# Kernel optimization log

Measured on AMD Instinct MI355X. Metric: run time of the kernel, lower is better.

## Reference

```python
import jax, jax.numpy as jnp
import numpy as np

N = 50000
E = 600000
F_IN = 128      # float features (in_channels - 1)
CE = 8          # cell embedding dim
D_IN = F_IN + CE  # 136
C = 128         # out_channels
NUM_CELLS = 854
NEG_SLOPE = 0.2
LN_EPS = 1e-5


def _gat_layer(x, src, dst, W, a_src, a_dst, b):
    """PyG GATConv, heads=1, concat=False, add_self_loops already in src/dst.
    x: [N, Din]; src/dst: [Etot]; W: [Din, C]; a_src/a_dst: [C]; b: [C].
    """
    h = x @ W                               # [N, C]
    alpha_src = h @ a_src                   # [N]
    alpha_dst = h @ a_dst                   # [N]
    e = jax.nn.leaky_relu(alpha_src[src] + alpha_dst[dst], NEG_SLOPE)  # [Etot]
    # segment softmax over edges sharing a destination node
    m = jax.ops.segment_max(e, dst, num_segments=N)    # [N] (every node has a self-loop)
    ex = jnp.exp(e - m[dst])                           # [Etot]
    denom = jax.ops.segment_sum(ex, dst, num_segments=N)  # [N]
    alpha = ex / denom[dst]                            # [Etot]
    out = jax.ops.segment_sum(h[src] * alpha[:, None], dst, num_segments=N)  # [N, C]
    return out + b


def _layer_norm(x, g, b):
    mu = jnp.mean(x, axis=-1, keepdims=True)
    var = jnp.var(x, axis=-1, keepdims=True)
    return (x - mu) * jax.lax.rsqrt(var + LN_EPS) * g + b


def setup_inputs() -> dict:
    key = jax.random.key(0)
    ks = jax.random.split(key, 12)
    x_base = jax.random.normal(ks[0], (N, F_IN), dtype=jnp.float32)
    cell_ids = jax.random.randint(ks[1], (N,), 0, NUM_CELLS, dtype=jnp.int64)
    edge_index = jax.random.randint(ks[2], (2, E), 0, N, dtype=jnp.int64)
    s = 0.05
    cell_emb = jax.random.normal(ks[3], (NUM_CELLS, CE), dtype=jnp.float32)
    W1 = jax.random.normal(ks[4], (D_IN, C), dtype=jnp.float32) * s
    a_src1 = jax.random.normal(ks[5], (C,), dtype=jnp.float32) * s
    a_dst1 = jax.random.normal(ks[6], (C,), dtype=jnp.float32) * s
    b1 = jnp.zeros((C,), dtype=jnp.float32)
    ln_g = jnp.ones((C,), dtype=jnp.float32)
    ln_b = jnp.zeros((C,), dtype=jnp.float32)
    W2 = jax.random.normal(ks[7], (C, C), dtype=jnp.float32) * s
    a_src2 = jax.random.normal(ks[8], (C,), dtype=jnp.float32) * s
    a_dst2 = jax.random.normal(ks[9], (C,), dtype=jnp.float32) * s
    b2 = jnp.zeros((C,), dtype=jnp.float32)
    return {
        "x_base": x_base, "cell_ids": cell_ids, "edge_index": edge_index,
        "cell_emb": cell_emb,
        "W1": W1, "a_src1": a_src1, "a_dst1": a_dst1, "b1": b1,
        "ln_g": ln_g, "ln_b": ln_b,
        "W2": W2, "a_src2": a_src2, "a_dst2": a_dst2, "b2": b2,
    }


def reference(x_base, cell_ids, edge_index, cell_emb,
              W1, a_src1, a_dst1, b1, ln_g, ln_b,
              W2, a_src2, a_dst2, b2):
    # embed cell ids and concat (equiv. to x[:, :-1] + Embedding(x[:, -1]))
    x = jnp.concatenate([x_base, cell_emb[cell_ids]], axis=1)   # [N, 136]
    # PyG GATConv adds self-loops internally
    loops = jnp.arange(N, dtype=edge_index.dtype)
    src = jnp.concatenate([edge_index[0], loops])
    dst = jnp.concatenate([edge_index[1], loops])
    # layer 1 + LN + ELU (dropout inactive in eval mode)
    x = _gat_layer(x, src, dst, W1, a_src1, a_dst1, b1)
    x = jax.nn.elu(_layer_norm(x, ln_g, ln_b))
    # layer 2 (no norm/activation on last layer)
    x = _gat_layer(x, src, dst, W2, a_src2, a_dst2, b2)
    return x
```

## Files before the change

kernel.cpp:

```cpp
#include <hip/hip_runtime.h>
#include <hip/hip_fp16.h>
#include <cstdint>
#include <cstddef>

#define NEG_SLOPE 0.2f
#define LN_EPS 1e-5f

constexpr int BS = 256;
constexpr int EPT = 8;
constexpr int SUBCAP = 96;
constexpr int STRIDE = 96;

typedef _Float16 f16x8 __attribute__((ext_vector_type(8)));
typedef float f32x4 __attribute__((ext_vector_type(4)));

__device__ __forceinline__ void agg_half8(
    const char* hbB, int idk, float wk, int qbase, int hoff, int l4, float acc[8])
{
    f16x8 hv[8];
    #pragma unroll
    for (int i = 0; i < 8; ++i) {
        int si = __shfl(idk, qbase + hoff + i);
        hv[i] = *(const f16x8*)(hbB + ((size_t)si << 8) + l4 * 16);
    }
    #pragma unroll
    for (int i = 0; i < 8; ++i) {
        float wi = __shfl(wk, qbase + hoff + i);
        #pragma unroll
        for (int c = 0; c < 8; ++c)
            acc[c] = fmaf(wi, (float)hv[i][c], acc[c]);
    }
}

__global__ __launch_bounds__(256) void k_init(
    const int* __restrict__ esrc, const int* __restrict__ edst,
    unsigned int* __restrict__ gb, int* __restrict__ bcnt,
    const float* __restrict__ W1, const float* __restrict__ W2,
    _Float16* __restrict__ Wt1, _Float16* __restrict__ Wt2,
    int e, int nb, int nblk)
{
    int b = blockIdx.x;
    if (b < nblk) {
        __shared__ int lcnt[64];
        int tid = threadIdx.x;
        if (tid < 64) lcnt[tid] = 0;
        __syncthreads();
        int base = b * (BS * EPT) + tid;
        int sv[EPT], dl[EPT], bk[EPT], lp[EPT];
        #pragma unroll
        for (int u = 0; u < EPT; ++u) {
            int i = base + u * BS;
            bool ok = i < e;
            int ii = ok ? i : 0;
            sv[u] = esrc[ii];
            int d = edst[ii];
            dl[u] = d & 1023;
            bk[u] = ok ? (d >> 10) : -1;
        }
        #pragma unroll
        for (int u = 0; u < EPT; ++u)
            lp[u] = (bk[u] >= 0) ? atomicAdd(&lcnt[bk[u]], 1) : SUBCAP;
        __syncthreads();
        if (tid < nb) bcnt[b * nb + tid] = lcnt[tid] < SUBCAP ? lcnt[tid] : SUBCAP;
        #pragma unroll
        for (int u = 0; u < EPT; ++u)
            if (bk[u] >= 0 && lp[u] < SUBCAP)
                gb[((size_t)bk[u] * nblk + b) * SUBCAP + lp[u]] =
                    ((unsigned)dl[u] << 16) | (unsigned)sv[u];
    } else {
        int idx = (b - nblk) * BS + threadIdx.x;
        if (idx < 128 * 160) {
            int nn = idx / 160, k = idx - nn * 160;
            Wt1[idx] = (_Float16)((k < 136) ? W1[(size_t)k * 128 + nn] : 0.f);
        } else if (idx < 128 * 160 + 128 * 128) {
            int j = idx - 128 * 160;
            int nn = j >> 7, k = j & 127;
            Wt2[j] = (_Float16)W2[(size_t)k * 128 + nn];
        }
    }
}

__global__ __launch_bounds__(256) void k_csr_gemm1(
    const unsigned int* __restrict__ gb, const int* __restrict__ bcnt,
    int* __restrict__ cnt, unsigned short* __restrict__ sn,
    const float* __restrict__ x, const int* __restrict__ cid,
    const float* __restrict__ emb,
    const _Float16* __restrict__ Wt1,
    const float* __restrict__ a_src, const float* __restrict__ a_dst,
    _Float16* __restrict__ hb, float* __restrict__ as_, float* __restrict__ ad_,
    int n, int nb, int nblk)
{
    __shared__ float red[2][16][2][2];
    __shared__ int cl[1024];
    int b = blockIdx.x;

    if (b < nb) {
        int tid = threadIdx.x;
        #pragma unroll 4
        for (int i = tid; i < 1024; i += BS) cl[i] = 1;
        __syncthreads();
        for (int blk = tid; blk < nblk; blk += BS) {
            int c = bcnt[blk * nb + b];
            size_t gbase = ((size_t)b * nblk + blk) * SUBCAP;
            for (int j = 0; j < c; j += 8) {
                uint4 p0 = *(const uint4*)(gb + gbase + j);
                uint4 p1 = *(const uint4*)(gb + gbase + j + 4);
                unsigned pk[8] = {p0.x, p0.y, p0.z, p0.w, p1.x, p1.y, p1.z, p1.w};
                int slot[8];
                #pragma unroll
                for (int k = 0; k < 8; ++k)
                    slot[k] = (j + k < c) ? atomicAdd(&cl[pk[k] >> 16], 1) : STRIDE;
                #pragma unroll
                for (int k = 0; k < 8; ++k)
                    if (slot[k] < STRIDE)
                        sn[((size_t)(b * 1024 + (int)(pk[k] >> 16))) * STRIDE + slot[k]] =
                            (unsigned short)(pk[k] & 0xFFFFu);
            }
        }
        __syncthreads();
        for (int i = tid; i < 1024; i += BS) {
            int node = b * 1024 + i;
            if (node < n) {
                int c = cl[i];
                cnt[node] = c < STRIDE ? c : STRIDE;
                sn[(size_t)node * STRIDE] = (unsigned short)node;
            }
        }
        return;
    }

    int idx = b - nb;
    int tid = threadIdx.x;
    int wave = tid >> 6, lane = tid & 63;
    int rg = wave >> 1, ch = wave & 1;
    int r15 = lane & 15, q = lane >> 4;
    int rowBase = idx * 32 + rg * 16;
    int colBase = ch * 64;
    int row = rowBase + r15;
    bool ok = row < n;
    int rl = ok ? row : n - 1;

    f32x4 acc[4] = {};
    const _Float16* Wp[4];
    #pragma unroll
    for (int s = 0; s < 4; ++s)
        Wp[s] = Wt1 + (size_t)(colBase + s * 16 + r15) * 160 + q * 8;
    const float* Xp = x + (size_t)rl * 128 + q * 8;

    #pragma unroll
    for (int k0 = 0; k0 < 128; k0 += 32) {
        f16x8 wv[4];
        #pragma unroll
        for (int s = 0; s < 4; ++s) wv[s] = *(const f16x8*)(Wp[s] + k0);
        float4 xlo = *(const float4*)(Xp + k0);
        float4 xhi = *(const float4*)(Xp + k0 + 4);
        f16x8 xv;
        xv[0] = (_Float16)xlo.x; xv[1] = (_Float16)xlo.y;
        xv[2] = (_Float16)xlo.z; xv[3] = (_Float16)xlo.w;
        xv[4] = (_Float16)xhi.x; xv[5] = (_Float16)xhi.y;
        xv[6] = (_Float16)xhi.z; xv[7] = (_Float16)xhi.w;
        #pragma unroll
        for (int s = 0; s < 4; ++s)
            acc[s] = __builtin_amdgcn_mfma_f32_16x16x32_f16(wv[s], xv, acc[s], 0, 0, 0);
    }
    {
        f16x8 wv[4];
        #pragma unroll
        for (int s = 0; s < 4; ++s) wv[s] = *(const f16x8*)(Wp[s] + 128);
        f16x8 xv;
        #pragma unroll
        for (int j = 0; j < 8; ++j) xv[j] = (_Float16)0.f;
        if (q == 0) {
            const float* er = emb + (size_t)cid[rl] * 8;
            float4 e0 = *(const float4*)er;
            float4 e1 = *(const float4*)(er + 4);
            xv[0] = (_Float16)e0.x; xv[1] = (_Float16)e0.y;
            xv[2] = (_Float16)e0.z; xv[3] = (_Float16)e0.w;
            xv[4] = (_Float16)e1.x; xv[5] = (_Float16)e1.y;
            xv[6] = (_Float16)e1.z; xv[7] = (_Float16)e1.w;
        }
        #pragma unroll
        for (int s = 0; s < 4; ++s)
            acc[s] = __builtin_amdgcn_mfma_f32_16x16x32_f16(wv[s], xv, acc[s], 0, 0, 0);
    }

    float vs = 0.f, vd = 0.f;
    #pragma unroll
    for (int s = 0; s < 4; ++s) {
        float4 as4 = *(const float4*)&a_src[colBase + s * 16 + q * 4];
        float4 ad4 = *(const float4*)&a_dst[colBase + s * 16 + q * 4];
        f32x4 d = acc[s];
        vs += d[0]*as4.x + d[1]*as4.y + d[2]*as4.z + d[3]*as4.w;
        vd += d[0]*ad4.x + d[1]*ad4.y + d[2]*ad4.z + d[3]*ad4.w;
        if (ok) {
            ushort4 u;
            u.x = __half_as_ushort(__float2half_rn(d[0]));
            u.y = __half_as_ushort(__float2half_rn(d[1]));
            u.z = __half_as_ushort(__float2half_rn(d[2]));
            u.w = __half_as_ushort(__float2half_rn(d[3]));
            *(ushort4*)&hb[(size_t)row * 128 + colBase + s * 16 + q * 4] = u;
        }
    }
    vs += __shfl_xor(vs, 16); vs += __shfl_xor(vs, 32);
    vd += __shfl_xor(vd, 16); vd += __shfl_xor(vd, 32);
    if (q == 0) { red[rg][r15][ch][0] = vs; red[rg][r15][ch][1] = vd; }
    __syncthreads();
    if (ch == 0 && q == 0 && ok) {
        as_[row] = red[rg][r15][0][0] + red[rg][r15][1][0];
        ad_[row] = red[rg][r15][0][1] + red[rg][r15][1][1];
    }
}

__global__ __launch_bounds__(512, 4) void k_agg1_gemm2(
    const _Float16* __restrict__ h1, const unsigned short* __restrict__ sn,
    const int* __restrict__ cnt, const float* __restrict__ as1,
    const float* __restrict__ ad1, const float* __restrict__ b1,
    const float* __restrict__ lng, const float* __restrict__ lnb,
    const _Float16* __restrict__ Wt2,
    const float* __restrict__ a_src2, const float* __restrict__ a_dst2,
    _Float16* __restrict__ h2, float* __restrict__ as2, float* __restrict__ ad2,
    int nn)
{
    __shared__ _Float16 yt[32][144];
    __shared__ float red[2][16][4][2];
    int t = blockIdx.x;
    int tid = threadIdx.x;
    int wave = tid >> 6, lane = tid & 63;
    int l4 = lane & 15, q = lane >> 4;
    int qg = wave * 4 + q;
    int node = t * 32 + qg;
    bool valid = node < nn;
    const char* hbB = (const char*)h1;
    int qbase = lane & 48;

    int len = 0; float adv = 0.f;
    if (valid) {
        len = cnt[node];
        len = len < STRIDE ? len : STRIDE;
        adv = ad1[node];
    }
    int start = valid ? node * STRIDE : 0;

    int id0 = sn[start + l4], id1 = sn[start + 16 + l4], id2 = sn[start + 32 + l4];
    id0 = (l4      < len) ? id0 : 0;
    id1 = (l4 + 16 < len) ? id1 : 0;
    id2 = (l4 + 32 < len) ? id2 : 0;
    float t0 = as1[id0] + adv; t0 = t0 > 0.f ? t0 : NEG_SLOPE * t0;
    float t1 = as1[id1] + adv; t1 = t1 > 0.f ? t1 : NEG_SLOPE * t1;
    float t2 = as1[id2] + adv; t2 = t2 > 0.f ? t2 : NEG_SLOPE * t2;
    float w0 = (l4      < len) ? __expf(fminf(t0, 70.f)) : 0.f;
    float w1 = (l4 + 16 < len) ? __expf(fminf(t1, 70.f)) : 0.f;
    float w2 = (l4 + 32 < len) ? __expf(fminf(t2, 70.f)) : 0.f;
    float wsum = w0 + w1 + w2;

    float acc[8] = {0.f, 0.f, 0.f, 0.f, 0.f, 0.f, 0.f, 0.f};
    agg_half8(hbB, id0, w0, qbase, 0, l4, acc);
    agg_half8(hbB, id0, w0, qbase, 8, l4, acc);
    if (len > 16) {
        agg_half8(hbB, id1, w1, qbase, 0, l4, acc);
        agg_half8(hbB, id1, w1, qbase, 8, l4, acc);
    }
    if (len > 32) {
        agg_half8(hbB, id2, w2, qbase, 0, l4, acc);
        agg_half8(hbB, id2, w2, qbase, 8, l4, acc);
    }
    for (int c = 48; c < len; c += 16) {
        int idk = sn[start + c + l4];
        bool a = (c + l4 < len);
        idk = a ? idk : 0;
        float tt = as1[idk] + adv; tt = tt > 0.f ? tt : NEG_SLOPE * tt;
        float wk = a ? __expf(fminf(tt, 70.f)) : 0.f;
        wsum += wk;
        agg_half8(hbB, idk, wk, qbase, 0, l4, acc);
        agg_half8(hbB, idk, wk, qbase, 8, l4, acc);
    }
    float dsum = wsum;
    dsum += __shfl_xor(dsum, 1); dsum += __shfl_xor(dsum, 2);
    dsum += __shfl_xor(dsum, 4); dsum += __shfl_xor(dsum, 8);

    if (valid) {
        float inv = 1.f / dsum;
        float4 b0 = *(const float4*)&b1[l4 * 8];
        float4 bb = *(const float4*)&b1[l4 * 8 + 4];
        float vv[8];
        vv[0] = acc[0] * inv + b0.x; vv[1] = acc[1] * inv + b0.y;
        vv[2] = acc[2] * inv + b0.z; vv[3] = acc[3] * inv + b0.w;
        vv[4] = acc[4] * inv + bb.x; vv[5] = acc[5] * inv + bb.y;
        vv[6] = acc[6] * inv + bb.z; vv[7] = acc[7] * inv + bb.w;

        float s1 = 0.f, s2 = 0.f;
        #pragma unroll
        for (int c = 0; c < 8; ++c) { s1 += vv[c]; s2 += vv[c] * vv[c]; }
        #pragma unroll
        for (int o = 1; o < 16; o <<= 1) {
            s1 += __shfl_xor(s1, o);
            s2 += __shfl_xor(s2, o);
        }
        float mean = s1 * (1.f / 128.f);
        float var  = s2 * (1.f / 128.f) - mean * mean;
        float r = rsqrtf(var + LN_EPS);
        float4 g0 = *(const float4*)&lng[l4 * 8];
        float4 g1 = *(const float4*)&lng[l4 * 8 + 4];
        float4 p0 = *(const float4*)&lnb[l4 * 8];
        float4 p1 = *(const float4*)&lnb[l4 * 8 + 4];
        float gg[8] = {g0.x, g0.y, g0.z, g0.w, g1.x, g1.y, g1.z, g1.w};
        float pp[8] = {p0.x, p0.y, p0.z, p0.w, p1.x, p1.y, p1.z, p1.w};
        f16x8 o;
        #pragma unroll
        for (int c = 0; c < 8; ++c) {
            float u = (vv[c] - mean) * r * gg[c] + pp[c];
            u = u > 0.f ? u : __expf(u) - 1.f;
            o[c] = (_Float16)u;
        }
        *(f16x8*)&yt[qg][l4 * 8] = o;
    } else {
        f16x8 z;
        #pragma unroll
        for (int c = 0; c < 8; ++c) z[c] = (_Float16)0.f;
        *(f16x8*)&yt[qg][l4 * 8] = z;
    }
    __syncthreads();

    int rg = wave >> 2, cc = wave & 3;
    int r15 = l4;
    int row = t * 32 + rg * 16 + r15;
    bool ok = row < nn;

    f32x4 acc2[2] = {};
    const _Float16* Wp[2];
    #pragma unroll
    for (int s = 0; s < 2; ++s)
        Wp[s] = Wt2 + (size_t)(cc * 32 + s * 16 + r15) * 128 + q * 8;
    const _Float16* Yp = &yt[rg * 16 + r15][q * 8];

    #pragma unroll
    for (int k0 = 0; k0 < 128; k0 += 32) {
        f16x8 wv[2];
        #pragma unroll
        for (int s = 0; s < 2; ++s) wv[s] = *(const f16x8*)(Wp[s] + k0);
        f16x8 xv = *(const f16x8*)(Yp + k0);
        #pragma unroll
        for (int s = 0; s < 2; ++s)
            acc2[s] = __builtin_amdgcn_mfma_f32_16x16x32_f16(wv[s], xv, acc2[s], 0, 0, 0);
    }

    float vs = 0.f, vd = 0.f;
    #pragma unroll
    for (int s = 0; s < 2; ++s) {
        float4 as4 = *(const float4*)&a_src2[cc * 32 + s * 16 + q * 4];
        float4 ad4 = *(const float4*)&a_dst2[cc * 32 + s * 16 + q * 4];
        f32x4 d = acc2[s];
        vs += d[0]*as4.x + d[1]*as4.y + d[2]*as4.z + d[3]*as4.w;
        vd += d[0]*ad4.x + d[1]*ad4.y + d[2]*ad4.z + d[3]*ad4.w;
        if (ok) {
            ushort4 u;
            u.x = __half_as_ushort(__float2half_rn(d[0]));
            u.y = __half_as_ushort(__float2half_rn(d[1]));
            u.z = __half_as_ushort(__float2half_rn(d[2]));
            u.w = __half_as_ushort(__float2half_rn(d[3]));
            *(ushort4*)&h2[(size_t)row * 128 + cc * 32 + s * 16 + q * 4] = u;
        }
    }
    vs += __shfl_xor(vs, 16); vs += __shfl_xor(vs, 32);
    vd += __shfl_xor(vd, 16); vd += __shfl_xor(vd, 32);
    if (q == 0) { red[rg][r15][cc][0] = vs; red[rg][r15][cc][1] = vd; }
    __syncthreads();
    if (cc == 0 && q == 0 && ok) {
        as2[row] = red[rg][r15][0][0] + red[rg][r15][1][0]
                 + red[rg][r15][2][0] + red[rg][r15][3][0];
        ad2[row] = red[rg][r15][0][1] + red[rg][r15][1][1]
                 + red[rg][r15][2][1] + red[rg][r15][3][1];
    }
}

__global__ __launch_bounds__(256, 4) void k_agg2(
    const _Float16* __restrict__ hb, const unsigned short* __restrict__ sn,
    const int* __restrict__ cnt, const float* __restrict__ as_,
    const float* __restrict__ ad_, const float* __restrict__ bias,
    float* __restrict__ out, int n_nodes)
{
    int tid = threadIdx.x;
    int wave = tid >> 6, lane = tid & 63;
    int l4 = lane & 15, q = lane >> 4;
    int node = blockIdx.x * 16 + wave * 4 + q;
    if (node >= n_nodes) return;
    int len = cnt[node];
    len = len < STRIDE ? len : STRIDE;
    int start = node * STRIDE;
    int qbase = lane & 48;
    float adv = ad_[node];
    const char* hbB = (const char*)hb;

    int id0 = sn[start + l4], id1 = sn[start + 16 + l4], id2 = sn[start + 32 + l4];
    id0 = (l4      < len) ? id0 : 0;
    id1 = (l4 + 16 < len) ? id1 : 0;
    id2 = (l4 + 32 < len) ? id2 : 0;
    float t0 = as_[id0] + adv; t0 = t0 > 0.f ? t0 : NEG_SLOPE * t0;
    float t1 = as_[id1] + adv; t1 = t1 > 0.f ? t1 : NEG_SLOPE * t1;
    float t2 = as_[id2] + adv; t2 = t2 > 0.f ? t2 : NEG_SLOPE * t2;
    float w0 = (l4      < len) ? __expf(fminf(t0, 70.f)) : 0.f;
    float w1 = (l4 + 16 < len) ? __expf(fminf(t1, 70.f)) : 0.f;
    float w2 = (l4 + 32 < len) ? __expf(fminf(t2, 70.f)) : 0.f;
    float wsum = w0 + w1 + w2;

    float acc[8] = {0.f, 0.f, 0.f, 0.f, 0.f, 0.f, 0.f, 0.f};
    agg_half8(hbB, id0, w0, qbase, 0, l4, acc);
    agg_half8(hbB, id0, w0, qbase, 8, l4, acc);
    if (len > 16) {
        agg_half8(hbB, id1, w1, qbase, 0, l4, acc);
        agg_half8(hbB, id1, w1, qbase, 8, l4, acc);
    }
    if (len > 32) {
        agg_half8(hbB, id2, w2, qbase, 0, l4, acc);
        agg_half8(hbB, id2, w2, qbase, 8, l4, acc);
    }
    for (int c = 48; c < len; c += 16) {
        int idk = sn[start + c + l4];
        bool a = (c + l4 < len);
        idk = a ? idk : 0;
        float tt = as_[idk] + adv; tt = tt > 0.f ? tt : NEG_SLOPE * tt;
        float wk = a ? __expf(fminf(tt, 70.f)) : 0.f;
        wsum += wk;
        agg_half8(hbB, idk, wk, qbase, 0, l4, acc);
        agg_half8(hbB, idk, wk, qbase, 8, l4, acc);
    }
    float dsum = wsum;
    dsum += __shfl_xor(dsum, 1); dsum += __shfl_xor(dsum, 2);
    dsum += __shfl_xor(dsum, 4); dsum += __shfl_xor(dsum, 8);

    float inv = 1.f / dsum;
    float4 b0 = *(const float4*)&bias[l4 * 8];
    float4 b1 = *(const float4*)&bias[l4 * 8 + 4];
    float4 o0 = make_float4(acc[0]*inv + b0.x, acc[1]*inv + b0.y,
                            acc[2]*inv + b0.z, acc[3]*inv + b0.w);
    float4 o1 = make_float4(acc[4]*inv + b1.x, acc[5]*inv + b1.y,
                            acc[6]*inv + b1.z, acc[7]*inv + b1.w);
    *(float4*)(out + (size_t)node * 128 + l4 * 8)     = o0;
    *(float4*)(out + (size_t)node * 128 + l4 * 8 + 4) = o1;
}


extern "C" void kernel_launch(void* const* d_in, const int* in_sizes, int n_in,
                              void* d_out, int out_size, void* d_ws, size_t ws_size,
                              hipStream_t stream) {
    const float* x_base   = (const float*)d_in[0];
    const int*   cell_ids = (const int*)d_in[1];
    const int*   eidx     = (const int*)d_in[2];
    const float* cell_emb = (const float*)d_in[3];
    const float* W1     = (const float*)d_in[4];
    const float* a_src1 = (const float*)d_in[5];
    const float* a_dst1 = (const float*)d_in[6];
    const float* b1     = (const float*)d_in[7];
    const float* ln_g   = (const float*)d_in[8];
    const float* ln_b   = (const float*)d_in[9];
    const float* W2     = (const float*)d_in[10];
    const float* a_src2 = (const float*)d_in[11];
    const float* a_dst2 = (const float*)d_in[12];
    const float* b2     = (const float*)d_in[13];

    const int N = in_sizes[0] / 128;
    const int E = in_sizes[2] / 2;

    const int* esrc = eidx;
    const int* edst = eidx + E;

    const int NB   = (N + 1023) >> 10;
    const int NBLK = (E + BS * EPT - 1) / (BS * EPT);

    auto align = [](size_t v) { return (v + 255) & ~(size_t)255; };
    char* p = (char*)d_ws;
    int*   cnt    = (int*)p;   p += align((size_t)N * 4);
    unsigned short* sn = (unsigned short*)p; p += align((size_t)N * STRIDE * 2 + 64);
    unsigned int* gb = (unsigned int*)p; p += align((size_t)NB * NBLK * SUBCAP * 4);
    int*   bcnt   = (int*)p;   p += align((size_t)NBLK * NB * 4);
    _Float16* h1  = (_Float16*)p; p += align((size_t)N * 128 * 2);
    _Float16* h2  = (_Float16*)p; p += align((size_t)N * 128 * 2);
    _Float16* Wt1 = (_Float16*)p; p += align((size_t)128 * 160 * 2);
    _Float16* Wt2 = (_Float16*)p; p += align((size_t)128 * 128 * 2);
    float* as1    = (float*)p; p += align((size_t)N * 4);
    float* ad1    = (float*)p; p += align((size_t)N * 4);
    float* as2    = (float*)p; p += align((size_t)N * 4);
    float* ad2    = (float*)p; p += align((size_t)N * 4);
    (void)ws_size; (void)n_in; (void)out_size;

    const int nbG = (N + 31) / 32;
    const int wblocks = (128 * 160 + 128 * 128 + BS - 1) / BS;

    k_init<<<NBLK + wblocks, BS, 0, stream>>>(
        esrc, edst, gb, bcnt, W1, W2, Wt1, Wt2, E, NB, NBLK);
    k_csr_gemm1<<<NB + nbG, BS, 0, stream>>>(
        gb, bcnt, cnt, sn, x_base, cell_ids, cell_emb, Wt1,
        a_src1, a_dst1, h1, as1, ad1, N, NB, NBLK);
    k_agg1_gemm2<<<nbG, 512, 0, stream>>>(
        h1, sn, cnt, as1, ad1, b1, ln_g, ln_b, Wt2,
        a_src2, a_dst2, h2, as2, ad2, N);
    k_agg2<<<(N + 15) / 16, BS, 0, stream>>>(
        h2, sn, cnt, as2, ad2, b2, (float*)d_out, N);
}
```

Baseline: 205.9 us.

## Sort nodes by degree within 1024-node chunks to balance aggregation waves

Each CSR-building block now builds a histogram of node in-degrees and counting-sorts its 1024 nodes by degree into a permutation array. The two aggregation kernels index nodes through this permutation, so the quarter-waves within a wave and block handle nodes of similar degree, which cuts divergence from per-lane loop lengths. In exchange it adds a serial prefix scan, shared-memory atomics and an extra indirection. It also scatters writes to h2/as2/ad2/out, losing contiguous row stores, and launches grids padded up to the chunk size.

```diff
diff --git a/kernel.cpp b/kernel.cpp
--- a/kernel.cpp
+++ b/kernel.cpp
@@ -10,6 +10,7 @@
 constexpr int EPT = 8;
 constexpr int SUBCAP = 96;
 constexpr int STRIDE = 96;
+constexpr int NBINS = 104;
 
 typedef _Float16 f16x8 __attribute__((ext_vector_type(8)));
 typedef float f32x4 __attribute__((ext_vector_type(4)));
@@ -83,6 +84,7 @@
 __global__ __launch_bounds__(256) void k_csr_gemm1(
     const unsigned int* __restrict__ gb, const int* __restrict__ bcnt,
     int* __restrict__ cnt, unsigned short* __restrict__ sn,
+    unsigned short* __restrict__ perm,
     const float* __restrict__ x, const int* __restrict__ cid,
     const float* __restrict__ emb,
     const _Float16* __restrict__ Wt1,
@@ -92,12 +94,15 @@
 {
     __shared__ float red[2][16][2][2];
     __shared__ int cl[1024];
+    __shared__ int hist[NBINS];
+    __shared__ int hbase[NBINS];
     int b = blockIdx.x;
 
     if (b < nb) {
         int tid = threadIdx.x;
         #pragma unroll 4
         for (int i = tid; i < 1024; i += BS) cl[i] = 1;
+        if (tid < NBINS) hist[tid] = 0;
         __syncthreads();
         for (int blk = tid; blk < nblk; blk += BS) {
             int c = bcnt[blk * nb + b];
@@ -120,11 +125,26 @@
         __syncthreads();
         for (int i = tid; i < 1024; i += BS) {
             int node = b * 1024 + i;
+            int c = cl[i];
+            int len = (node < n) ? (c < STRIDE ? c : STRIDE) : 0;
             if (node < n) {
-                int c = cl[i];
-                cnt[node] = c < STRIDE ? c : STRIDE;
+                cnt[node] = len;
                 sn[(size_t)node * STRIDE] = (unsigned short)node;
             }
+            atomicAdd(&hist[len], 1);
+        }
+        __syncthreads();
+        if (tid == 0) {
+            int run = 0;
+            for (int k = 0; k < NBINS; ++k) { hbase[k] = run; run += hist[k]; }
+        }
+        __syncthreads();
+        for (int i = tid; i < 1024; i += BS) {
+            int node = b * 1024 + i;
+            int c = cl[i];
+            int len = (node < n) ? (c < STRIDE ? c : STRIDE) : 0;
+            int pos = atomicAdd(&hbase[len], 1);
+            perm[b * 1024 + pos] = (node < n) ? (unsigned short)node : (unsigned short)0xFFFF;
         }
         return;
     }
@@ -213,7 +233,8 @@
 
 __global__ __launch_bounds__(512, 4) void k_agg1_gemm2(
     const _Float16* __restrict__ h1, const unsigned short* __restrict__ sn,
-    const int* __restrict__ cnt, const float* __restrict__ as1,
+    const int* __restrict__ cnt, const unsigned short* __restrict__ perm,
+    const float* __restrict__ as1,
     const float* __restrict__ ad1, const float* __restrict__ b1,
     const float* __restrict__ lng, const float* __restrict__ lnb,
     const _Float16* __restrict__ Wt2,
@@ -228,7 +249,7 @@
     int wave = tid >> 6, lane = tid & 63;
     int l4 = lane & 15, q = lane >> 4;
     int qg = wave * 4 + q;
-    int node = t * 32 + qg;
+    int node = perm[t * 32 + qg];
     bool valid = node < nn;
     const char* hbB = (const char*)h1;
     int qbase = lane & 48;
@@ -323,8 +344,8 @@
 
     int rg = wave >> 2, cc = wave & 3;
     int r15 = l4;
-    int row = t * 32 + rg * 16 + r15;
-    bool ok = row < nn;
+    int onode = perm[t * 32 + rg * 16 + r15];
+    bool ok = onode < nn;
 
     f32x4 acc2[2] = {};
     const _Float16* Wp[2];
@@ -358,7 +379,7 @@
             u.y = __half_as_ushort(__float2half_rn(d[1]));
             u.z = __half_as_ushort(__float2half_rn(d[2]));
             u.w = __half_as_ushort(__float2half_rn(d[3]));
-            *(ushort4*)&h2[(size_t)row * 128 + cc * 32 + s * 16 + q * 4] = u;
+            *(ushort4*)&h2[(size_t)onode * 128 + cc * 32 + s * 16 + q * 4] = u;
         }
     }
     vs += __shfl_xor(vs, 16); vs += __shfl_xor(vs, 32);
@@ -366,23 +387,24 @@
     if (q == 0) { red[rg][r15][cc][0] = vs; red[rg][r15][cc][1] = vd; }
     __syncthreads();
     if (cc == 0 && q == 0 && ok) {
-        as2[row] = red[rg][r15][0][0] + red[rg][r15][1][0]
-                 + red[rg][r15][2][0] + red[rg][r15][3][0];
-        ad2[row] = red[rg][r15][0][1] + red[rg][r15][1][1]
-                 + red[rg][r15][2][1] + red[rg][r15][3][1];
+        as2[onode] = red[rg][r15][0][0] + red[rg][r15][1][0]
+                   + red[rg][r15][2][0] + red[rg][r15][3][0];
+        ad2[onode] = red[rg][r15][0][1] + red[rg][r15][1][1]
+                   + red[rg][r15][2][1] + red[rg][r15][3][1];
     }
 }
 
 __global__ __launch_bounds__(256, 4) void k_agg2(
     const _Float16* __restrict__ hb, const unsigned short* __restrict__ sn,
-    const int* __restrict__ cnt, const float* __restrict__ as_,
+    const int* __restrict__ cnt, const unsigned short* __restrict__ perm,
+    const float* __restrict__ as_,
     const float* __restrict__ ad_, const float* __restrict__ bias,
     float* __restrict__ out, int n_nodes)
 {
     int tid = threadIdx.x;
     int wave = tid >> 6, lane = tid & 63;
     int l4 = lane & 15, q = lane >> 4;
-    int node = blockIdx.x * 16 + wave * 4 + q;
+    int node = perm[blockIdx.x * 16 + wave * 4 + q];
     if (node >= n_nodes) return;
     int len = cnt[node];
     len = len < STRIDE ? len : STRIDE;
@@ -466,11 +488,13 @@
 
     const int NB   = (N + 1023) >> 10;
     const int NBLK = (E + BS * EPT - 1) / (BS * EPT);
+    const int PN   = NB * 1024;
 
     auto align = [](size_t v) { return (v + 255) & ~(size_t)255; };
     char* p = (char*)d_ws;
     int*   cnt    = (int*)p;   p += align((size_t)N * 4);
     unsigned short* sn = (unsigned short*)p; p += align((size_t)N * STRIDE * 2 + 64);
+    unsigned short* perm = (unsigned short*)p; p += align((size_t)PN * 2);
     unsigned int* gb = (unsigned int*)p; p += align((size_t)NB * NBLK * SUBCAP * 4);
     int*   bcnt   = (int*)p;   p += align((size_t)NBLK * NB * 4);
     _Float16* h1  = (_Float16*)p; p += align((size_t)N * 128 * 2);
@@ -489,11 +513,11 @@
     k_init<<<NBLK + wblocks, BS, 0, stream>>>(
         esrc, edst, gb, bcnt, W1, W2, Wt1, Wt2, E, NB, NBLK);
     k_csr_gemm1<<<NB + nbG, BS, 0, stream>>>(
-        gb, bcnt, cnt, sn, x_base, cell_ids, cell_emb, Wt1,
+        gb, bcnt, cnt, sn, perm, x_base, cell_ids, cell_emb, Wt1,
         a_src1, a_dst1, h1, as1, ad1, N, NB, NBLK);
-    k_agg1_gemm2<<<nbG, 512, 0, stream>>>(
-        h1, sn, cnt, as1, ad1, b1, ln_g, ln_b, Wt2,
+    k_agg1_gemm2<<<PN / 32, 512, 0, stream>>>(
+        h1, sn, cnt, perm, as1, ad1, b1, ln_g, ln_b, Wt2,
         a_src2, a_dst2, h2, as2, ad2, N);
-    k_agg2<<<(N + 15) / 16, BS, 0, stream>>>(
-        h2, sn, cnt, as2, ad2, b2, (float*)d_out, N);
+    k_agg2<<<PN / 16, BS, 0, stream>>>(
+        h2, sn, cnt, perm, as2, ad2, b2, (float*)d_out, N);
 }
```

Measured after the change: 211.5 us. 2.7% more time.

## Split neighbor feature gather into two half-row passes separated by a block barrier

Applied to the files above, without the earlier changes.

Both aggregation kernels now gather each neighbor's 256-byte fp16 row in two passes, first bytes 0-127 then bytes 128-255, using 8-byte loads per lane instead of 16-byte loads. A __syncthreads separates the passes, presumably so the block's working set per pass fits better in cache or L2, or so waves stay in step. The cost is recomputing edge weights and indices in the tail loop and issuing twice as many smaller loads. k_agg2 no longer returns early for out-of-range nodes, which keeps the barrier safe for all threads.

```diff
diff --git a/kernel.cpp b/kernel.cpp
--- a/kernel.cpp
+++ b/kernel.cpp
@@ -12,22 +12,23 @@
 constexpr int STRIDE = 96;
 
 typedef _Float16 f16x8 __attribute__((ext_vector_type(8)));
+typedef _Float16 f16x4 __attribute__((ext_vector_type(4)));
 typedef float f32x4 __attribute__((ext_vector_type(4)));
 
-__device__ __forceinline__ void agg_half8(
-    const char* hbB, int idk, float wk, int qbase, int hoff, int l4, float acc[8])
+__device__ __forceinline__ void agg_slice8(
+    const char* hbB, int idk, float wk, int qbase, int hoff, int byteoff, float acc[4])
 {
-    f16x8 hv[8];
+    f16x4 hv[8];
     #pragma unroll
     for (int i = 0; i < 8; ++i) {
         int si = __shfl(idk, qbase + hoff + i);
-        hv[i] = *(const f16x8*)(hbB + ((size_t)si << 8) + l4 * 16);
+        hv[i] = *(const f16x4*)(hbB + ((size_t)si << 8) + byteoff);
     }
     #pragma unroll
     for (int i = 0; i < 8; ++i) {
         float wi = __shfl(wk, qbase + hoff + i);
         #pragma unroll
-        for (int c = 0; c < 8; ++c)
+        for (int c = 0; c < 4; ++c)
             acc[c] = fmaf(wi, (float)hv[i][c], acc[c]);
     }
 }
@@ -253,16 +254,20 @@
     float w2 = (l4 + 32 < len) ? __expf(fminf(t2, 70.f)) : 0.f;
     float wsum = w0 + w1 + w2;
 
-    float acc[8] = {0.f, 0.f, 0.f, 0.f, 0.f, 0.f, 0.f, 0.f};
-    agg_half8(hbB, id0, w0, qbase, 0, l4, acc);
-    agg_half8(hbB, id0, w0, qbase, 8, l4, acc);
+    int offA = l4 * 8;
+    int offB = 128 + l4 * 8;
+    float accA[4] = {0.f, 0.f, 0.f, 0.f};
+    float accB[4] = {0.f, 0.f, 0.f, 0.f};
+
+    agg_slice8(hbB, id0, w0, qbase, 0, offA, accA);
+    agg_slice8(hbB, id0, w0, qbase, 8, offA, accA);
     if (len > 16) {
-        agg_half8(hbB, id1, w1, qbase, 0, l4, acc);
-        agg_half8(hbB, id1, w1, qbase, 8, l4, acc);
+        agg_slice8(hbB, id1, w1, qbase, 0, offA, accA);
+        agg_slice8(hbB, id1, w1, qbase, 8, offA, accA);
     }
     if (len > 32) {
-        agg_half8(hbB, id2, w2, qbase, 0, l4, acc);
-        agg_half8(hbB, id2, w2, qbase, 8, l4, acc);
+        agg_slice8(hbB, id2, w2, qbase, 0, offA, accA);
+        agg_slice8(hbB, id2, w2, qbase, 8, offA, accA);
     }
     for (int c = 48; c < len; c += 16) {
         int idk = sn[start + c + l4];
@@ -271,22 +276,43 @@
         float tt = as1[idk] + adv; tt = tt > 0.f ? tt : NEG_SLOPE * tt;
         float wk = a ? __expf(fminf(tt, 70.f)) : 0.f;
         wsum += wk;
-        agg_half8(hbB, idk, wk, qbase, 0, l4, acc);
-        agg_half8(hbB, idk, wk, qbase, 8, l4, acc);
-    }
+        agg_slice8(hbB, idk, wk, qbase, 0, offA, accA);
+        agg_slice8(hbB, idk, wk, qbase, 8, offA, accA);
+    }
+    __syncthreads();
+    agg_slice8(hbB, id0, w0, qbase, 0, offB, accB);
+    agg_slice8(hbB, id0, w0, qbase, 8, offB, accB);
+    if (len > 16) {
+        agg_slice8(hbB, id1, w1, qbase, 0, offB, accB);
+        agg_slice8(hbB, id1, w1, qbase, 8, offB, accB);
+    }
+    if (len > 32) {
+        agg_slice8(hbB, id2, w2, qbase, 0, offB, accB);
+        agg_slice8(hbB, id2, w2, qbase, 8, offB, accB);
+    }
+    for (int c = 48; c < len; c += 16) {
+        int idk = sn[start + c + l4];
+        bool a = (c + l4 < len);
+        idk = a ? idk : 0;
+        float tt = as1[idk] + adv; tt = tt > 0.f ? tt : NEG_SLOPE * tt;
+        float wk = a ? __expf(fminf(tt, 70.f)) : 0.f;
+        agg_slice8(hbB, idk, wk, qbase, 0, offB, accB);
+        agg_slice8(hbB, idk, wk, qbase, 8, offB, accB);
+    }
+
     float dsum = wsum;
     dsum += __shfl_xor(dsum, 1); dsum += __shfl_xor(dsum, 2);
     dsum += __shfl_xor(dsum, 4); dsum += __shfl_xor(dsum, 8);
 
     if (valid) {
         float inv = 1.f / dsum;
-        float4 b0 = *(const float4*)&b1[l4 * 8];
-        float4 bb = *(const float4*)&b1[l4 * 8 + 4];
+        float4 bA = *(const float4*)&b1[l4 * 4];
+        float4 bB = *(const float4*)&b1[64 + l4 * 4];
         float vv[8];
-        vv[0] = acc[0] * inv + b0.x; vv[1] = acc[1] * inv + b0.y;
-        vv[2] = acc[2] * inv + b0.z; vv[3] = acc[3] * inv + b0.w;
-        vv[4] = acc[4] * inv + bb.x; vv[5] = acc[5] * inv + bb.y;
-        vv[6] = acc[6] * inv + bb.z; vv[7] = acc[7] * inv + bb.w;
+        vv[0] = accA[0] * inv + bA.x; vv[1] = accA[1] * inv + bA.y;
+        vv[2] = accA[2] * inv + bA.z; vv[3] = accA[3] * inv + bA.w;
+        vv[4] = accB[0] * inv + bB.x; vv[5] = accB[1] * inv + bB.y;
+        vv[6] = accB[2] * inv + bB.z; vv[7] = accB[3] * inv + bB.w;
 
         float s1 = 0.f, s2 = 0.f;
         #pragma unroll
@@ -299,25 +325,27 @@
         float mean = s1 * (1.f / 128.f);
         float var  = s2 * (1.f / 128.f) - mean * mean;
         float r = rsqrtf(var + LN_EPS);
-        float4 g0 = *(const float4*)&lng[l4 * 8];
-        float4 g1 = *(const float4*)&lng[l4 * 8 + 4];
-        float4 p0 = *(const float4*)&lnb[l4 * 8];
-        float4 p1 = *(const float4*)&lnb[l4 * 8 + 4];
-        float gg[8] = {g0.x, g0.y, g0.z, g0.w, g1.x, g1.y, g1.z, g1.w};
-        float pp[8] = {p0.x, p0.y, p0.z, p0.w, p1.x, p1.y, p1.z, p1.w};
-        f16x8 o;
+        float4 gA = *(const float4*)&lng[l4 * 4];
+        float4 gB = *(const float4*)&lng[64 + l4 * 4];
+        float4 pA = *(const float4*)&lnb[l4 * 4];
+        float4 pB = *(const float4*)&lnb[64 + l4 * 4];
+        float gg[8] = {gA.x, gA.y, gA.z, gA.w, gB.x, gB.y, gB.z, gB.w};
+        float pp[8] = {pA.x, pA.y, pA.z, pA.w, pB.x, pB.y, pB.z, pB.w};
+        f16x4 oA, oB;
         #pragma unroll
         for (int c = 0; c < 8; ++c) {
             float u = (vv[c] - mean) * r * gg[c] + pp[c];
             u = u > 0.f ? u : __expf(u) - 1.f;
-            o[c] = (_Float16)u;
-        }
-        *(f16x8*)&yt[qg][l4 * 8] = o;
+            if (c < 4) oA[c] = (_Float16)u; else oB[c - 4] = (_Float16)u;
+        }
+        *(f16x4*)&yt[qg][l4 * 4]      = oA;
+        *(f16x4*)&yt[qg][64 + l4 * 4] = oB;
     } else {
-        f16x8 z;
-        #pragma unroll
-        for (int c = 0; c < 8; ++c) z[c] = (_Float16)0.f;
-        *(f16x8*)&yt[qg][l4 * 8] = z;
+        f16x4 z;
+        #pragma unroll
+        for (int c = 0; c < 4; ++c) z[c] = (_Float16)0.f;
+        *(f16x4*)&yt[qg][l4 * 4]      = z;
+        *(f16x4*)&yt[qg][64 + l4 * 4] = z;
     }
     __syncthreads();
 
@@ -383,12 +411,15 @@
     int wave = tid >> 6, lane = tid & 63;
     int l4 = lane & 15, q = lane >> 4;
     int node = blockIdx.x * 16 + wave * 4 + q;
-    if (node >= n_nodes) return;
-    int len = cnt[node];
-    len = len < STRIDE ? len : STRIDE;
-    int start = node * STRIDE;
+    bool valid = node < n_nodes;
+    int len = 0; float adv = 0.f;
+    if (valid) {
+        len = cnt[node];
+        len = len < STRIDE ? len : STRIDE;
+        adv = ad_[node];
+    }
+    int start = valid ? node * STRIDE : 0;
     int qbase = lane & 48;
-    float adv = ad_[node];
     const char* hbB = (const char*)hb;
 
     int id0 = sn[start + l4], id1 = sn[start + 16 + l4], id2 = sn[start + 32 + l4];
@@ -403,16 +434,20 @@
     float w2 = (l4 + 32 < len) ? __expf(fminf(t2, 70.f)) : 0.f;
     float wsum = w0 + w1 + w2;
 
-    float acc[8] = {0.f, 0.f, 0.f, 0.f, 0.f, 0.f, 0.f, 0.f};
-    agg_half8(hbB, id0, w0, qbase, 0, l4, acc);
-    agg_half8(hbB, id0, w0, qbase, 8, l4, acc);
+    int offA = l4 * 8;
+    int offB = 128 + l4 * 8;
+    float accA[4] = {0.f, 0.f, 0.f, 0.f};
+    float accB[4] = {0.f, 0.f, 0.f, 0.f};
+
+    agg_slice8(hbB, id0, w0, qbase, 0, offA, accA);
+    agg_slice8(hbB, id0, w0, qbase, 8, offA, accA);
     if (len > 16) {
-        agg_half8(hbB, id1, w1, qbase, 0, l4, acc);
-        agg_half8(hbB, id1, w1, qbase, 8, l4, acc);
+        agg_slice8(hbB, id1, w1, qbase, 0, offA, accA);
+        agg_slice8(hbB, id1, w1, qbase, 8, offA, accA);
     }
     if (len > 32) {
-        agg_half8(hbB, id2, w2, qbase, 0, l4, acc);
-        agg_half8(hbB, id2, w2, qbase, 8, l4, acc);
+        agg_slice8(hbB, id2, w2, qbase, 0, offA, accA);
+        agg_slice8(hbB, id2, w2, qbase, 8, offA, accA);
     }
     for (int c = 48; c < len; c += 16) {
         int idk = sn[start + c + l4];
@@ -421,22 +456,45 @@
         float tt = as_[idk] + adv; tt = tt > 0.f ? tt : NEG_SLOPE * tt;
         float wk = a ? __expf(fminf(tt, 70.f)) : 0.f;
         wsum += wk;
-        agg_half8(hbB, idk, wk, qbase, 0, l4, acc);
-        agg_half8(hbB, idk, wk, qbase, 8, l4, acc);
-    }
+        agg_slice8(hbB, idk, wk, qbase, 0, offA, accA);
+        agg_slice8(hbB, idk, wk, qbase, 8, offA, accA);
+    }
+    __syncthreads();
+    agg_slice8(hbB, id0, w0, qbase, 0, offB, accB);
+    agg_slice8(hbB, id0, w0, qbase, 8, offB, accB);
+    if (len > 16) {
+        agg_slice8(hbB, id1, w1, qbase, 0, offB, accB);
+        agg_slice8(hbB, id1, w1, qbase, 8, offB, accB);
+    }
+    if (len > 32) {
+        agg_slice8(hbB, id2, w2, qbase, 0, offB, accB);
+        agg_slice8(hbB, id2, w2, qbase, 8, offB, accB);
+    }
+    for (int c = 48; c < len; c += 16) {
+        int idk = sn[start + c + l4];
+        bool a = (c + l4 < len);
+        idk = a ? idk : 0;
+        float tt = as_[idk] + adv; tt = tt > 0.f ? tt : NEG_SLOPE * tt;
+        float wk = a ? __expf(fminf(tt, 70.f)) : 0.f;
+        agg_slice8(hbB, idk, wk, qbase, 0, offB, accB);
+        agg_slice8(hbB, idk, wk, qbase, 8, offB, accB);
+    }
+
     float dsum = wsum;
     dsum += __shfl_xor(dsum, 1); dsum += __shfl_xor(dsum, 2);
     dsum += __shfl_xor(dsum, 4); dsum += __shfl_xor(dsum, 8);
 
-    float inv = 1.f / dsum;
-    float4 b0 = *(const float4*)&bias[l4 * 8];
-    float4 b1 = *(const float4*)&bias[l4 * 8 + 4];
-    float4 o0 = make_float4(acc[0]*inv + b0.x, acc[1]*inv + b0.y,
-                            acc[2]*inv + b0.z, acc[3]*inv + b0.w);
-    float4 o1 = make_float4(acc[4]*inv + b1.x, acc[5]*inv + b1.y,
-                            acc[6]*inv + b1.z, acc[7]*inv + b1.w);
-    *(float4*)(out + (size_t)node * 128 + l4 * 8)     = o0;
-    *(float4*)(out + (size_t)node * 128 + l4 * 8 + 4) = o1;
+    if (valid) {
+        float inv = 1.f / dsum;
+        float4 bA = *(const float4*)&bias[l4 * 4];
+        float4 bB = *(const float4*)&bias[64 + l4 * 4];
+        float4 oA = make_float4(accA[0]*inv + bA.x, accA[1]*inv + bA.y,
+                                accA[2]*inv + bA.z, accA[3]*inv + bA.w);
+        float4 oB = make_float4(accB[0]*inv + bB.x, accB[1]*inv + bB.y,
+                                accB[2]*inv + bB.z, accB[3]*inv + bB.w);
+        *(float4*)(out + (size_t)node * 128 + l4 * 4)      = oA;
+        *(float4*)(out + (size_t)node * 128 + 64 + l4 * 4) = oB;
+    }
 }
 
 
```

New measurement: 215.5 us. +4.6%, slower.
